# Kernel optimization log

Measured on AMD Instinct MI355X. Metric: run time of the kernel, lower is better.

Reference implementation:

```python
import itertools
import jax, jax.numpy as jnp
import numpy as np

B, RES, RES_, STRIDE = 512, 14, 7, 2
IN_DIM, OUT_DIM, KEY_DIM, H, ATTN_RATIO = 256, 512, 16, 8, 2
NH_KD = KEY_DIM * H          # 128
D = ATTN_RATIO * KEY_DIM     # 32
DH = D * H                   # 256
KV_OUT = DH + NH_KD          # 384
N, N_ = RES * RES, RES_ * RES_   # 196, 49
EPS = 1e-5
SCALE = KEY_DIM ** -0.5


def _build_bias_idxs():
    points = list(itertools.product(range(RES), range(RES)))
    points_ = list(itertools.product(range(RES_), range(RES_)))
    offsets, idxs = {}, []
    for p1 in points_:
        for p2 in points:
            off = (abs(p1[0] * STRIDE - p2[0]), abs(p1[1] * STRIDE - p2[1]))
            if off not in offsets:
                offsets[off] = len(offsets)
            idxs.append(offsets[off])
    return np.array(idxs, dtype=np.int32).reshape(N_, N), len(offsets)


def _bn(x, g, b, m, v):
    # inference-mode BatchNorm1d over last dim
    return (x - m) * (g * jax.lax.rsqrt(v + EPS)) + b


def _hardswish(x):
    return x * jnp.clip(x + 3.0, 0.0, 6.0) * (1.0 / 6.0)


def setup_inputs() -> dict:
    key = jax.random.key(0)
    ks = jax.random.split(key, 16)
    idxs_np, n_off = _build_bias_idxs()
    inp = {
        "x": jax.random.normal(ks[0], (B, N, IN_DIM), jnp.float32),
        "w_kv": jax.random.normal(ks[1], (KV_OUT, IN_DIM), jnp.float32) * 0.02,
        "kv_g": jnp.ones((KV_OUT,), jnp.float32),
        "kv_b": jax.random.normal(ks[2], (KV_OUT,), jnp.float32) * 0.01,
        "kv_m": jax.random.normal(ks[3], (KV_OUT,), jnp.float32) * 0.01,
        "kv_v": jax.random.uniform(ks[4], (KV_OUT,), jnp.float32) + 0.5,
        "w_q": jax.random.normal(ks[5], (NH_KD, IN_DIM), jnp.float32) * 0.02,
        "q_g": jnp.ones((NH_KD,), jnp.float32),
        "q_b": jax.random.normal(ks[6], (NH_KD,), jnp.float32) * 0.01,
        "q_m": jax.random.normal(ks[7], (NH_KD,), jnp.float32) * 0.01,
        "q_v": jax.random.uniform(ks[8], (NH_KD,), jnp.float32) + 0.5,
        "w_p": jax.random.normal(ks[9], (OUT_DIM, DH), jnp.float32) * 0.02,
        "p_g": jnp.ones((OUT_DIM,), jnp.float32),
        "p_b": jax.random.normal(ks[10], (OUT_DIM,), jnp.float32) * 0.01,
        "p_m": jax.random.normal(ks[11], (OUT_DIM,), jnp.float32) * 0.01,
        "p_v": jax.random.uniform(ks[12], (OUT_DIM,), jnp.float32) + 0.5,
        "ab_table": jax.random.normal(ks[13], (H, n_off), jnp.float32) * 0.02,
        "bias_idxs": jnp.asarray(idxs_np),  # [N_, N] int32
    }
    return inp


def reference(x, w_kv, kv_g, kv_b, kv_m, kv_v,
              w_q, q_g, q_b, q_m, q_v,
              w_p, p_g, p_b, p_m, p_v,
              ab_table, bias_idxs):
    Bx = x.shape[0]
    # kv projection: [B, N, KV_OUT] -> split heads into k [B,H,N,KEY_DIM], v [B,H,N,D]
    kv = _bn(jnp.einsum('bnc,oc->bno', x, w_kv), kv_g, kv_b, kv_m, kv_v)
    kv = kv.reshape(Bx, N, H, KEY_DIM + D)
    k = kv[..., :KEY_DIM].transpose(0, 2, 1, 3)   # [B,H,N,KEY_DIM]
    v = kv[..., KEY_DIM:].transpose(0, 2, 1, 3)   # [B,H,N,D]
    # query path: spatial subsample then Linear+BN
    xs = x.reshape(Bx, RES, RES, IN_DIM)[:, ::STRIDE, ::STRIDE].reshape(Bx, N_, IN_DIM)
    q = _bn(jnp.einsum('bnc,oc->bno', xs, w_q), q_g, q_b, q_m, q_v)
    q = q.reshape(Bx, N_, H, KEY_DIM).transpose(0, 2, 1, 3)  # [B,H,N_,KEY_DIM]
    # relative-position bias gather: [H, N_, N]
    ab = ab_table[:, bias_idxs]
    attn = jnp.einsum('bhqd,bhkd->bhqk', q, k) * SCALE + ab
    attn = jax.nn.softmax(attn, axis=-1)
    out = jnp.einsum('bhqk,bhkd->bhqd', attn, v)           # [B,H,N_,D]
    out = out.transpose(0, 2, 1, 3).reshape(Bx, N_, DH)
    out = _hardswish(out)
    out = _bn(jnp.einsum('bnd,od->bno', out, w_p), p_g, p_b, p_m, p_v)
    return out
```

## Files before the change

### kernel.cpp

```cpp
#include <hip/hip_runtime.h>

typedef __attribute__((ext_vector_type(8))) short bf16x8;
typedef __attribute__((ext_vector_type(4))) float f32x4;
typedef __attribute__((ext_vector_type(4))) short short4v;
typedef __attribute__((ext_vector_type(4))) unsigned int u32x4;
typedef __attribute__((ext_vector_type(2))) unsigned int u32x2;

#define DEVFN static __device__ __forceinline__

DEVFN short f2bf(float f) {
  unsigned int u = __builtin_bit_cast(unsigned int, f);
  unsigned int r = (u + 0x7FFFu + ((u >> 16) & 1u)) >> 16;
  return (short)r;
}

DEVFN unsigned int pack2bf(float a, float b) {
  unsigned int lo = (unsigned int)(unsigned short)f2bf(a);
  unsigned int hi = (unsigned int)(unsigned short)f2bf(b);
  return lo | (hi << 16);
}

DEVFN f32x4 mfma_bf16(bf16x8 a, bf16x8 b, f32x4 c) {
  return __builtin_amdgcn_mfma_f32_16x16x32_bf16(a, b, c, 0, 0, 0);
}

DEVFN f32x4 zero4() { f32x4 z = {0.f, 0.f, 0.f, 0.f}; return z; }
DEVFN bf16x8 zero8() { bf16x8 z = {0,0,0,0,0,0,0,0}; return z; }

DEVFN void gload_lds16(const void* g, void* l) {
  __builtin_amdgcn_global_load_lds(
      (const __attribute__((address_space(1))) unsigned int*)g,
      (__attribute__((address_space(3))) unsigned int*)l, 16, 0, 0);
}

DEVFN bf16x8 lds8(const short* p) {
  short4v lo = *reinterpret_cast<const short4v*>(p);
  short4v hi = *reinterpret_cast<const short4v*>(p + 4);
  bf16x8 r;
  r[0] = lo[0]; r[1] = lo[1]; r[2] = lo[2]; r[3] = lo[3];
  r[4] = hi[0]; r[5] = hi[1]; r[6] = hi[2]; r[7] = hi[3];
  return r;
}

DEVFN bf16x8 cvt8v(float4 u0, float4 u1) {
  bf16x8 r;
  r[0] = f2bf(u0.x); r[1] = f2bf(u0.y); r[2] = f2bf(u0.z); r[3] = f2bf(u0.w);
  r[4] = f2bf(u1.x); r[5] = f2bf(u1.y); r[6] = f2bf(u1.z); r[7] = f2bf(u1.w);
  return r;
}

DEVFN float bfhi2f(unsigned int hi16) {
  return __builtin_bit_cast(float, hi16 << 16);
}
DEVFN float bfhi2f_hi(unsigned int word) {
  return __builtin_bit_cast(float, word & 0xffff0000u);
}

DEVFN void pack_w_body(const float* __restrict__ w, const float* __restrict__ g,
                       const float* __restrict__ b, const float* __restrict__ m,
                       const float* __restrict__ v, short* __restrict__ pk,
                       float* __restrict__ bias, int O, int t) {
  const int nt = O >> 4;
  const int total = nt * 8 * 64;
  if (t < total) {
    int lane = t & 63;
    int j = (t >> 6) % nt;
    int c = (t >> 6) / nt;
    int row = j * 16 + (lane & 15);
    int col = c * 32 + (lane >> 4) * 8;
    float s = g[row] * rsqrtf(v[row] + 1e-5f);
    const float* wp = w + (size_t)row * 256 + col;
    short* o = pk + (size_t)t * 8;
#pragma unroll
    for (int e = 0; e < 8; ++e) o[e] = f2bf(wp[e] * s);
  }
  if (t < O) {
    float s = g[t] * rsqrtf(v[t] + 1e-5f);
    bias[t] = b[t] - m[t] * s;
  }
}

__global__ __launch_bounds__(256) void prologue_k(
    const float* __restrict__ w_kv, const float* __restrict__ kv_g,
    const float* __restrict__ kv_b, const float* __restrict__ kv_m,
    const float* __restrict__ kv_v, short* __restrict__ pk_kv,
    float* __restrict__ bs_kv,
    const float* __restrict__ w_q, const float* __restrict__ q_g,
    const float* __restrict__ q_b, const float* __restrict__ q_m,
    const float* __restrict__ q_v, short* __restrict__ pk_q,
    float* __restrict__ bs_q,
    const float* __restrict__ w_p, const float* __restrict__ p_g,
    const float* __restrict__ p_b, const float* __restrict__ p_m,
    const float* __restrict__ p_v, short* __restrict__ pk_p,
    float* __restrict__ bs_p,
    const float* __restrict__ tab, const int* __restrict__ idxs,
    u32x2* __restrict__ ab3, int n_off) {
  const int blk = blockIdx.x, tid = threadIdx.x;
  if (blk < 48) {
    pack_w_body(w_kv, kv_g, kv_b, kv_m, kv_v, pk_kv, bs_kv, 384, blk * 256 + tid);
  } else if (blk < 64) {
    pack_w_body(w_q, q_g, q_b, q_m, q_v, pk_q, bs_q, 128, (blk - 48) * 256 + tid);
  } else if (blk < 128) {
    pack_w_body(w_p, p_g, p_b, p_m, p_v, pk_p, bs_p, 512, (blk - 64) * 256 + tid);
  } else {
    const int vb = (blk - 128) * 4 + (tid >> 6);
    const int lane = tid & 63;
    if (vb < 416) {
      const int t = vb % 13, w = (vb / 13) & 3, h = vb / 52;
      const int l15 = lane & 15, g = lane >> 4;
      int q = w * 16 + l15; if (q > 48) q = 48;
      const int nb = (t >> 1) * 32 + g * 8 + (t & 1) * 4;
      u32x2 out; out[0] = 0u; out[1] = 0u;
      if (nb < 196) {
        const int* irow = idxs + q * 196 + nb;
        const float* th = tab + h * n_off;
        out[0] = pack2bf(th[irow[0]], th[irow[1]]);
        out[1] = pack2bf(th[irow[2]], th[irow[3]]);
      }
      ab3[(size_t)vb * 64 + lane] = out;
    }
  }
}

__global__ __launch_bounds__(512, 4) void kvq_k(
    const float* __restrict__ x,
    const short* __restrict__ pk_kv, const float* __restrict__ bs_kv,
    short* __restrict__ k_out, short* __restrict__ vT_out,
    const short* __restrict__ pk_q, const float* __restrict__ bs_q,
    short* __restrict__ q_out) {
  __shared__ short smem[16640];
  const int tid = threadIdx.x, w = tid >> 6, lane = tid & 63;
  const int l15 = lane & 15, g = lane >> 4;

  if (blockIdx.x < 1568) {
    short* xs2 = smem;
    const int mt = blockIdx.x;
    const float* xb = x + (size_t)mt * 64 * 256;
#pragma unroll
    for (int it = 0; it < 4; ++it) {
      int i = it * 512 + tid;
      int row = i >> 5, gc = i & 31;
      const float* src = xb + row * 256 + gc * 8;
      float4 u0 = *reinterpret_cast<const float4*>(src);
      float4 u1 = *reinterpret_cast<const float4*>(src + 4);
      *reinterpret_cast<bf16x8*>(reinterpret_cast<char*>(xs2) + row * 512 +
                                 ((gc * 16) ^ ((row & 7) << 4))) = cvt8v(u0, u1);
    }
    __syncthreads();

    f32x4 acc[4][3];
#pragma unroll
    for (int m = 0; m < 4; ++m) {
      acc[m][0] = zero4(); acc[m][1] = zero4(); acc[m][2] = zero4();
    }
    const int swz = (l15 & 7) << 4;
#pragma unroll
    for (int c = 0; c < 8; ++c) {
      bf16x8 wf0 = *reinterpret_cast<const bf16x8*>(pk_kv + ((size_t)(c * 24 + 3 * w) * 64 + lane) * 8);
      bf16x8 wf1 = *reinterpret_cast<const bf16x8*>(pk_kv + ((size_t)(c * 24 + 3 * w + 1) * 64 + lane) * 8);
      bf16x8 wf2 = *reinterpret_cast<const bf16x8*>(pk_kv + ((size_t)(c * 24 + 3 * w + 2) * 64 + lane) * 8);
#pragma unroll
      for (int m = 0; m < 4; ++m) {
        const int row = m * 16 + l15;
        bf16x8 a = *reinterpret_cast<const bf16x8*>(
            reinterpret_cast<const char*>(xs2) + row * 512 +
            ((c * 64 + g * 16) ^ swz));
        acc[m][0] = mfma_bf16(a, wf0, acc[m][0]);
        acc[m][1] = mfma_bf16(a, wf1, acc[m][1]);
        acc[m][2] = mfma_bf16(a, wf2, acc[m][2]);
      }
    }

    const float bvK = bs_kv[(3 * w) * 16 + l15];
    const float bv1 = bs_kv[(3 * w + 1) * 16 + l15];
    const float bv2 = bs_kv[(3 * w + 2) * 16 + l15];
#pragma unroll
    for (int m = 0; m < 4; ++m) {
      const int row0 = mt * 64 + m * 16 + g * 4;
      const int bb_ = row0 / 196, n0 = row0 % 196;
      short* kp = k_out + ((size_t)(bb_ * 8 + w) * 196 + n0) * 16 + l15;
#pragma unroll
      for (int r = 0; r < 4; ++r) kp[r * 16] = f2bf(acc[m][0][r] + bvK);
      short4v sv;
#pragma unroll
      for (int r = 0; r < 4; ++r) sv[r] = f2bf(acc[m][1][r] + bv1);
      *reinterpret_cast<short4v*>(
          vT_out + ((size_t)(bb_ * 8 + w) * 32 + l15) * 196 + n0) = sv;
#pragma unroll
      for (int r = 0; r < 4; ++r) sv[r] = f2bf(acc[m][2][r] + bv2);
      *reinterpret_cast<short4v*>(
          vT_out + ((size_t)(bb_ * 8 + w) * 32 + 16 + l15) * 196 + n0) = sv;
    }
  } else {
    short* bs = smem;
    float* sb = reinterpret_cast<float*>(smem + 4096);
    const int mt = blockIdx.x - 1568;
    if (tid < 128) sb[tid] = bs_q[tid];
    const int arow = mt * 128 + w * 16 + l15;
    const int b = arow / 49, qi = arow % 49;
    const int n = 28 * (qi / 7) + 2 * (qi % 7);
    const float* xrow = x + ((size_t)b * 196 + n) * 256;

    f32x4 acc[8];
#pragma unroll
    for (int j = 0; j < 8; ++j) acc[j] = zero4();

    for (int c = 0; c < 8; ++c) {
      gload_lds16(pk_q + ((size_t)(c * 8 + w) * 64 + lane) * 8, &bs[w * 512]);
      const float4 u0 = *reinterpret_cast<const float4*>(xrow + c * 32 + g * 8);
      const float4 u1 = *reinterpret_cast<const float4*>(xrow + c * 32 + g * 8 + 4);
      bf16x8 a = cvt8v(u0, u1);
      __syncthreads();
#pragma unroll
      for (int j = 0; j < 8; ++j) {
        bf16x8 bj = *reinterpret_cast<const bf16x8*>(&bs[(j * 64 + lane) * 8]);
        acc[j] = mfma_bf16(a, bj, acc[j]);
      }
      __syncthreads();
    }
    const int orow = mt * 128 + w * 16 + g * 4;
#pragma unroll
    for (int j = 0; j < 8; ++j) {
      int ch = j * 16 + l15;
      float bb = sb[ch];
#pragma unroll
      for (int r = 0; r < 4; ++r)
        q_out[(size_t)(orow + r) * 128 + ch] = f2bf(acc[j][r] + bb);
    }
  }
}

__global__ __launch_bounds__(256) void attn4_k(
    const short* __restrict__ k_ws, const short* __restrict__ vT_ws,
    const short* __restrict__ qw, const u32x2* __restrict__ ab3,
    short* __restrict__ out) {
  __shared__ short vt[6304];
  __shared__ short kst[3200];
  const int b = blockIdx.x >> 3, h = blockIdx.x & 7;
  const int tid = threadIdx.x, w_id = tid >> 6, lane = tid & 63;
  const int l15 = lane & 15, g = lane >> 4;

  if (tid < 16) *reinterpret_cast<unsigned int*>(&vt[6272 + tid * 2]) = 0u;

  const short* vsrc = vT_ws + (size_t)(b * 8 + h) * 6272;
  for (int s = w_id; s < 13; s += 4) {
    if (s * 64 + lane < 784)
      gload_lds16(vsrc + (size_t)(s * 64 + lane) * 8, &vt[s * 512]);
  }
  const short* ksrc = k_ws + (size_t)(b * 8 + h) * 3136;
  for (int s = w_id; s < 7; s += 4) {
    if (s * 64 + lane < 392)
      gload_lds16(ksrc + (size_t)(s * 64 + lane) * 8, &kst[s * 512]);
  }

  const int q = w_id * 16 + l15;
  const bool qok = q < 49;
  bf16x8 bq = zero8();
  if (g < 2 && qok)
    bq = *reinterpret_cast<const bf16x8*>(
        qw + ((size_t)b * 49 + q) * 128 + h * 16 + g * 8);

  __syncthreads();

  f32x4 s[13];
#pragma unroll
  for (int t = 0; t < 13; ++t) {
    int n_a = (t >> 1) * 32 + (l15 >> 2) * 8 + (t & 1) * 4 + (l15 & 3);
    bf16x8 ak = zero8();
    if (g < 2 && n_a < 196) ak = lds8(&kst[n_a * 16 + g * 8]);
    s[t] = mfma_bf16(ak, bq, zero4());
  }

  const u32x2* abp = ab3 + (size_t)((h * 4 + w_id) * 13) * 64 + lane;
#pragma unroll
  for (int t = 0; t < 13; ++t) {
    int nb = (t >> 1) * 32 + g * 8 + (t & 1) * 4;
    if (nb < 196) {
      u32x2 bv = abp[t * 64];
      s[t][0] = s[t][0] * 0.25f + bfhi2f(bv[0]);
      s[t][1] = s[t][1] * 0.25f + bfhi2f_hi(bv[0]);
      s[t][2] = s[t][2] * 0.25f + bfhi2f(bv[1]);
      s[t][3] = s[t][3] * 0.25f + bfhi2f_hi(bv[1]);
    } else {
      s[t][0] = -1e30f; s[t][1] = -1e30f; s[t][2] = -1e30f; s[t][3] = -1e30f;
    }
  }

  float mx = s[0][0];
#pragma unroll
  for (int t = 0; t < 13; ++t)
    mx = fmaxf(mx, fmaxf(fmaxf(s[t][0], s[t][1]), fmaxf(s[t][2], s[t][3])));
  mx = fmaxf(mx, __shfl_xor(mx, 16, 64));
  mx = fmaxf(mx, __shfl_xor(mx, 32, 64));
  float sum = 0.f;
#pragma unroll
  for (int t = 0; t < 13; ++t) {
#pragma unroll
    for (int r = 0; r < 4; ++r) {
      float e = __expf(s[t][r] - mx);
      s[t][r] = e;
      sum += e;
    }
  }
  sum += __shfl_xor(sum, 16, 64);
  sum += __shfl_xor(sum, 32, 64);
  const float inv = 1.f / sum;

  unsigned int pkr[14][2];
#pragma unroll
  for (int t = 0; t < 13; ++t) {
    pkr[t][0] = pack2bf(s[t][0] * inv, s[t][1] * inv);
    pkr[t][1] = pack2bf(s[t][2] * inv, s[t][3] * inv);
  }
  pkr[13][0] = 0u; pkr[13][1] = 0u;

  f32x4 o0 = zero4(), o1 = zero4();
#pragma unroll
  for (int c = 0; c < 7; ++c) {
    u32x4 bp_u;
    bp_u[0] = pkr[2 * c][0];     bp_u[1] = pkr[2 * c][1];
    bp_u[2] = pkr[2 * c + 1][0]; bp_u[3] = pkr[2 * c + 1][1];
    bf16x8 bp = __builtin_bit_cast(bf16x8, bp_u);
    bf16x8 a0 = lds8(&vt[l15 * 196 + c * 32 + g * 8]);
    bf16x8 a1 = lds8(&vt[(16 + l15) * 196 + c * 32 + g * 8]);
    o0 = mfma_bf16(a0, bp, o0);
    o1 = mfma_bf16(a1, bp, o1);
  }

  if (qok) {
    short* op = out + (((size_t)b * 49 + q) * 256 + h * 32 + g * 4);
    short4v v0, v1;
#pragma unroll
    for (int r = 0; r < 4; ++r) {
      float x0 = o0[r];
      v0[r] = f2bf(x0 * fminf(fmaxf(x0 + 3.f, 0.f), 6.f) * (1.f / 6.f));
      float x1 = o1[r];
      v1[r] = f2bf(x1 * fminf(fmaxf(x1 + 3.f, 0.f), 6.f) * (1.f / 6.f));
    }
    *reinterpret_cast<short4v*>(op) = v0;
    *reinterpret_cast<short4v*>(op + 16) = v1;
  }
}

__global__ void p_gemm3(
    const short* __restrict__ a_in, const short* __restrict__ pk,
    const float* __restrict__ bias, float* __restrict__ out) {
  __shared__ short as_[32 * 256];
  const int tid = threadIdx.x, w = tid >> 6, lane = tid & 63;
  const int l15 = lane & 15, g = lane >> 4;
  const int half = blockIdx.x & 1;
  const int mt = blockIdx.x >> 1;

  const short* ab_ = a_in + (size_t)mt * 32 * 256;
#pragma unroll
  for (int it = 0; it < 4; ++it) {
    int i = it * 256 + tid;
    int row = i >> 5, gc = i & 31;
    bf16x8 vv = *reinterpret_cast<const bf16x8*>(ab_ + row * 256 + gc * 8);
    *reinterpret_cast<bf16x8*>(reinterpret_cast<char*>(as_) + row * 512 +
                               ((gc * 16) ^ ((row & 7) << 4))) = vv;
  }
  __syncthreads();

  f32x4 acc[2][4];
#pragma unroll
  for (int m = 0; m < 2; ++m)
#pragma unroll
    for (int jj = 0; jj < 4; ++jj) acc[m][jj] = zero4();

  const int jbase = half * 16 + w * 4;
#pragma unroll
  for (int c = 0; c < 8; ++c) {
    bf16x8 wf[4];
#pragma unroll
    for (int jj = 0; jj < 4; ++jj)
      wf[jj] = *reinterpret_cast<const bf16x8*>(
          pk + ((size_t)(c * 32 + jbase + jj) * 64 + lane) * 8);
#pragma unroll
    for (int m = 0; m < 2; ++m) {
      const int row = m * 16 + l15;
      bf16x8 a = *reinterpret_cast<const bf16x8*>(
          reinterpret_cast<const char*>(as_) + row * 512 +
          ((c * 64 + g * 16) ^ ((row & 7) << 4)));
#pragma unroll
      for (int jj = 0; jj < 4; ++jj)
        acc[m][jj] = mfma_bf16(a, wf[jj], acc[m][jj]);
    }
  }

#pragma unroll
  for (int m = 0; m < 2; ++m) {
    const int row0 = mt * 32 + m * 16 + g * 4;
#pragma unroll
    for (int jj = 0; jj < 4; ++jj) {
      const int och = (jbase + jj) * 16 + l15;
      const float bv = bias[och];
#pragma unroll
      for (int r = 0; r < 4; ++r)
        out[(size_t)(row0 + r) * 512 + och] = acc[m][jj][r] + bv;
    }
  }
}

extern "C" void kernel_launch(void* const* d_in, const int* in_sizes, int n_in,
                              void* d_out, int out_size, void* d_ws, size_t ws_size,
                              hipStream_t stream) {
  const float* x    = (const float*)d_in[0];
  const float* w_kv = (const float*)d_in[1];
  const float* kv_g = (const float*)d_in[2];
  const float* kv_b = (const float*)d_in[3];
  const float* kv_m = (const float*)d_in[4];
  const float* kv_v = (const float*)d_in[5];
  const float* w_q  = (const float*)d_in[6];
  const float* q_g  = (const float*)d_in[7];
  const float* q_b  = (const float*)d_in[8];
  const float* q_m  = (const float*)d_in[9];
  const float* q_v  = (const float*)d_in[10];
  const float* w_p  = (const float*)d_in[11];
  const float* p_g  = (const float*)d_in[12];
  const float* p_b  = (const float*)d_in[13];
  const float* p_m  = (const float*)d_in[14];
  const float* p_v  = (const float*)d_in[15];
  const float* ab_t = (const float*)d_in[16];
  const int*   idxs = (const int*)d_in[17];
  const int n_off = in_sizes[16] / 8;

  char* ws = (char*)d_ws;
  short* pk_kv  = (short*)(ws);
  short* pk_q   = (short*)(ws + 196608);
  short* pk_p   = (short*)(ws + 262144);
  float* bs_kv  = (float*)(ws + 524288);
  float* bs_q   = (float*)(ws + 525824);
  float* bs_p   = (float*)(ws + 526336);
  u32x2* ab3_ws = (u32x2*)(ws + 528384);
  short* k_ws   = (short*)(ws + 835712);
  short* vT_ws  = (short*)(ws + 26525824);
  short* q_ws   = (short*)(ws + 77906048);
  short* at_ws  = (short*)(ws + 84328576);

  prologue_k<<<dim3(232), dim3(256), 0, stream>>>(
      w_kv, kv_g, kv_b, kv_m, kv_v, pk_kv, bs_kv,
      w_q, q_g, q_b, q_m, q_v, pk_q, bs_q,
      w_p, p_g, p_b, p_m, p_v, pk_p, bs_p,
      ab_t, idxs, ab3_ws, n_off);

  kvq_k<<<dim3(1764), dim3(512), 0, stream>>>(
      x, pk_kv, bs_kv, k_ws, vT_ws, pk_q, bs_q, q_ws);
  attn4_k<<<dim3(4096), dim3(256), 0, stream>>>(k_ws, vT_ws, q_ws, ab3_ws, at_ws);
  p_gemm3<<<dim3(1568), dim3(256), 0, stream>>>(at_ws, pk_p, bs_p, (float*)d_out);
}
```

Measured before the change: 114.7 us.

## Process two KV row tiles per block with register-prefetched second tile

Each KV-projection block now handles two 64-row tiles instead of one, halving the KV block count. The second tile's fp32 input is loaded into registers while the MFMA work for the first tile runs, so global load latency overlaps with compute. The cost is extra registers for the prefetched data, which may lower occupancy, and fewer blocks for the scheduler to spread across the GPU.

```diff
diff --git a/kernel.cpp b/kernel.cpp
--- a/kernel.cpp
+++ b/kernel.cpp
@@ -132,69 +132,109 @@
   const int tid = threadIdx.x, w = tid >> 6, lane = tid & 63;
   const int l15 = lane & 15, g = lane >> 4;
 
-  if (blockIdx.x < 1568) {
+  if (blockIdx.x < 784) {
     short* xs2 = smem;
-    const int mt = blockIdx.x;
-    const float* xb = x + (size_t)mt * 64 * 256;
+    const int swz = (l15 & 7) << 4;
+
+    auto compute_and_store = [&](int mt) {
+      f32x4 acc[4][3];
+#pragma unroll
+      for (int m = 0; m < 4; ++m) {
+        acc[m][0] = zero4(); acc[m][1] = zero4(); acc[m][2] = zero4();
+      }
+#pragma unroll
+      for (int c = 0; c < 8; ++c) {
+        bf16x8 wf0 = *reinterpret_cast<const bf16x8*>(pk_kv + ((size_t)(c * 24 + 3 * w) * 64 + lane) * 8);
+        bf16x8 wf1 = *reinterpret_cast<const bf16x8*>(pk_kv + ((size_t)(c * 24 + 3 * w + 1) * 64 + lane) * 8);
+        bf16x8 wf2 = *reinterpret_cast<const bf16x8*>(pk_kv + ((size_t)(c * 24 + 3 * w + 2) * 64 + lane) * 8);
+#pragma unroll
+        for (int m = 0; m < 4; ++m) {
+          const int row = m * 16 + l15;
+          bf16x8 a = *reinterpret_cast<const bf16x8*>(
+              reinterpret_cast<const char*>(xs2) + row * 512 +
+              ((c * 64 + g * 16) ^ swz));
+          acc[m][0] = mfma_bf16(a, wf0, acc[m][0]);
+          acc[m][1] = mfma_bf16(a, wf1, acc[m][1]);
+          acc[m][2] = mfma_bf16(a, wf2, acc[m][2]);
+        }
+      }
+      const float bvK = bs_kv[(3 * w) * 16 + l15];
+      const float bv1 = bs_kv[(3 * w + 1) * 16 + l15];
+      const float bv2 = bs_kv[(3 * w + 2) * 16 + l15];
+#pragma unroll
+      for (int m = 0; m < 4; ++m) {
+        const int row0 = mt * 64 + m * 16 + g * 4;
+        const int bb_ = row0 / 196, n0 = row0 % 196;
+        short* kp = k_out + ((size_t)(bb_ * 8 + w) * 196 + n0) * 16 + l15;
+#pragma unroll
+        for (int r = 0; r < 4; ++r) kp[r * 16] = f2bf(acc[m][0][r] + bvK);
+        short4v sv;
+#pragma unroll
+        for (int r = 0; r < 4; ++r) sv[r] = f2bf(acc[m][1][r] + bv1);
+        *reinterpret_cast<short4v*>(
+            vT_out + ((size_t)(bb_ * 8 + w) * 32 + l15) * 196 + n0) = sv;
+#pragma unroll
+        for (int r = 0; r < 4; ++r) sv[r] = f2bf(acc[m][2][r] + bv2);
+        *reinterpret_cast<short4v*>(
+            vT_out + ((size_t)(bb_ * 8 + w) * 32 + 16 + l15) * 196 + n0) = sv;
+      }
+    };
+
+    const int mtA = blockIdx.x * 2, mtB = mtA + 1;
+
+    {
+      const float* xbA = x + (size_t)mtA * 64 * 256;
+      float4 a0[4], a1[4];
+#pragma unroll
+      for (int it = 0; it < 4; ++it) {
+        int i = it * 512 + tid;
+        int row = i >> 5, gc = i & 31;
+        const float* src = xbA + row * 256 + gc * 8;
+        a0[it] = *reinterpret_cast<const float4*>(src);
+        a1[it] = *reinterpret_cast<const float4*>(src + 4);
+      }
+#pragma unroll
+      for (int it = 0; it < 4; ++it) {
+        int i = it * 512 + tid;
+        int row = i >> 5, gc = i & 31;
+        *reinterpret_cast<bf16x8*>(reinterpret_cast<char*>(xs2) + row * 512 +
+                                   ((gc * 16) ^ ((row & 7) << 4))) =
+            cvt8v(a0[it], a1[it]);
+      }
+    }
+    __syncthreads();
+
+    float4 b0[4], b1[4];
+    {
+      const float* xbB = x + (size_t)mtB * 64 * 256;
+#pragma unroll
+      for (int it = 0; it < 4; ++it) {
+        int i = it * 512 + tid;
+        int row = i >> 5, gc = i & 31;
+        const float* src = xbB + row * 256 + gc * 8;
+        b0[it] = *reinterpret_cast<const float4*>(src);
+        b1[it] = *reinterpret_cast<const float4*>(src + 4);
+      }
+    }
+
+    compute_and_store(mtA);
+    __syncthreads();
+
 #pragma unroll
     for (int it = 0; it < 4; ++it) {
       int i = it * 512 + tid;
       int row = i >> 5, gc = i & 31;
-      const float* src = xb + row * 256 + gc * 8;
-      float4 u0 = *reinterpret_cast<const float4*>(src);
-      float4 u1 = *reinterpret_cast<const float4*>(src + 4);
       *reinterpret_cast<bf16x8*>(reinterpret_cast<char*>(xs2) + row * 512 +
-                                 ((gc * 16) ^ ((row & 7) << 4))) = cvt8v(u0, u1);
+                                 ((gc * 16) ^ ((row & 7) << 4))) =
+          cvt8v(b0[it], b1[it]);
     }
     __syncthreads();
 
-    f32x4 acc[4][3];
-#pragma unroll
-    for (int m = 0; m < 4; ++m) {
-      acc[m][0] = zero4(); acc[m][1] = zero4(); acc[m][2] = zero4();
-    }
-    const int swz = (l15 & 7) << 4;
-#pragma unroll
-    for (int c = 0; c < 8; ++c) {
-      bf16x8 wf0 = *reinterpret_cast<const bf16x8*>(pk_kv + ((size_t)(c * 24 + 3 * w) * 64 + lane) * 8);
-      bf16x8 wf1 = *reinterpret_cast<const bf16x8*>(pk_kv + ((size_t)(c * 24 + 3 * w + 1) * 64 + lane) * 8);
-      bf16x8 wf2 = *reinterpret_cast<const bf16x8*>(pk_kv + ((size_t)(c * 24 + 3 * w + 2) * 64 + lane) * 8);
-#pragma unroll
-      for (int m = 0; m < 4; ++m) {
-        const int row = m * 16 + l15;
-        bf16x8 a = *reinterpret_cast<const bf16x8*>(
-            reinterpret_cast<const char*>(xs2) + row * 512 +
-            ((c * 64 + g * 16) ^ swz));
-        acc[m][0] = mfma_bf16(a, wf0, acc[m][0]);
-        acc[m][1] = mfma_bf16(a, wf1, acc[m][1]);
-        acc[m][2] = mfma_bf16(a, wf2, acc[m][2]);
-      }
-    }
-
-    const float bvK = bs_kv[(3 * w) * 16 + l15];
-    const float bv1 = bs_kv[(3 * w + 1) * 16 + l15];
-    const float bv2 = bs_kv[(3 * w + 2) * 16 + l15];
-#pragma unroll
-    for (int m = 0; m < 4; ++m) {
-      const int row0 = mt * 64 + m * 16 + g * 4;
-      const int bb_ = row0 / 196, n0 = row0 % 196;
-      short* kp = k_out + ((size_t)(bb_ * 8 + w) * 196 + n0) * 16 + l15;
-#pragma unroll
-      for (int r = 0; r < 4; ++r) kp[r * 16] = f2bf(acc[m][0][r] + bvK);
-      short4v sv;
-#pragma unroll
-      for (int r = 0; r < 4; ++r) sv[r] = f2bf(acc[m][1][r] + bv1);
-      *reinterpret_cast<short4v*>(
-          vT_out + ((size_t)(bb_ * 8 + w) * 32 + l15) * 196 + n0) = sv;
-#pragma unroll
-      for (int r = 0; r < 4; ++r) sv[r] = f2bf(acc[m][2][r] + bv2);
-      *reinterpret_cast<short4v*>(
-          vT_out + ((size_t)(bb_ * 8 + w) * 32 + 16 + l15) * 196 + n0) = sv;
-    }
+    compute_and_store(mtB);
   } else {
     short* bs = smem;
     float* sb = reinterpret_cast<float*>(smem + 4096);
-    const int mt = blockIdx.x - 1568;
+    const int mt = blockIdx.x - 784;
     if (tid < 128) sb[tid] = bs_q[tid];
     const int arow = mt * 128 + w * 16 + l15;
     const int b = arow / 49, qi = arow % 49;
@@ -444,7 +484,7 @@
       w_p, p_g, p_b, p_m, p_v, pk_p, bs_p,
       ab_t, idxs, ab3_ws, n_off);
 
-  kvq_k<<<dim3(1764), dim3(512), 0, stream>>>(
+  kvq_k<<<dim3(980), dim3(512), 0, stream>>>(
       x, pk_kv, bs_kv, k_ws, vT_ws, pk_q, bs_q, q_ws);
   attn4_k<<<dim3(4096), dim3(256), 0, stream>>>(k_ws, vT_ws, q_ws, ab3_ws, at_ws);
   p_gemm3<<<dim3(1568), dim3(256), 0, stream>>>(at_ws, pk_p, bs_p, (float*)d_out);
```

Measured after the change: 120.1 us. +4.7%, slower.
